# Kernel optimization log

Hardware: AMD Instinct MI355X
Metric: run time of the kernel (lower is better)

The kernel has to match this reference:

```python
import jax, jax.numpy as jnp
import numpy as np

IOU_THRESHOLD = 0.5
NEG_POS_RATIO = 3
CENTER_VARIANCE = 0.1
SIZE_VARIANCE = 0.2


def _corner_to_center(b):
    return jnp.concatenate([(b[..., :2] + b[..., 2:]) * 0.5, b[..., 2:] - b[..., :2]], axis=-1)


def _area(lt, rb):
    wh = jnp.clip(rb - lt, 0.0)
    return wh[..., 0] * wh[..., 1]


def _iou(boxes0, boxes1, eps=1e-5):
    lt = jnp.maximum(boxes0[..., :2], boxes1[..., :2])
    rb = jnp.minimum(boxes0[..., 2:], boxes1[..., 2:])
    inter = _area(lt, rb)
    a0 = _area(boxes0[..., :2], boxes0[..., 2:])
    a1 = _area(boxes1[..., :2], boxes1[..., 2:])
    return inter / (a0 + a1 - inter + eps)


def _match_one(gt_boxes, gt_labels, valid, anchors_corner, anchors_center):
    # gt_boxes [G,4] corner, gt_labels [G], valid [G] bool, anchors [A,4]
    G = gt_boxes.shape[0]
    A = anchors_corner.shape[0]
    ious = _iou(gt_boxes[:, None, :], anchors_corner[None, :, :])  # [G, A]
    ious = jnp.where(valid[:, None], ious, -1.0)  # mask padded gts
    best_target_iou = ious.max(axis=0)            # [A]
    best_target_idx = ious.argmax(axis=0)         # [A]
    best_prior_idx = ious.argmax(axis=1)          # [G]
    # force-assign each valid gt to its best anchor (invalid rows -> OOB, dropped)
    safe_prior = jnp.where(valid, best_prior_idx, A)
    best_target_idx = best_target_idx.at[safe_prior].set(jnp.arange(G), mode='drop')
    best_target_iou = best_target_iou.at[safe_prior].set(2.0, mode='drop')
    labels = jnp.where(best_target_iou < IOU_THRESHOLD, 0, gt_labels[best_target_idx])
    boxes_c = _corner_to_center(gt_boxes[best_target_idx])  # [A,4] center form
    loc = jnp.concatenate([
        (boxes_c[:, :2] - anchors_center[:, :2]) / anchors_center[:, 2:] / CENTER_VARIANCE,
        jnp.log(jnp.clip(boxes_c[:, 2:] / anchors_center[:, 2:], 1e-8)) / SIZE_VARIANCE,
    ], axis=-1)
    return labels, loc


def _multibox_loss(confidence, predicted_locations, gts, counts, anchors):
    B, A, C = confidence.shape
    G = gts.shape[1]
    gt_boxes = gts[..., :4]
    gt_labels = gts[..., 4].astype(jnp.int32)
    valid = jnp.arange(G)[None, :] < counts[:, None]  # [B, G]
    anchors_center = _corner_to_center(anchors)
    labels, gt_locations = jax.vmap(_match_one, in_axes=(0, 0, 0, None, None))(
        gt_boxes, gt_labels, valid, anchors, anchors_center)  # [B,A], [B,A,4]

    log_probs = jax.nn.log_softmax(confidence, axis=2)  # [B, A, C]
    bg_loss = -log_probs[:, :, 0]                       # [B, A]
    pos_mask = labels > 0
    num_pos_row = pos_mask.sum(axis=1, keepdims=True)   # [B, 1]
    # hard negative mining: rank background losses per row, keep top 3*num_pos
    mining = jnp.where(pos_mask, -jnp.inf, bg_loss)
    order = jnp.argsort(-mining, axis=1)
    rank = jnp.argsort(order, axis=1)
    neg_mask = rank < num_pos_row * NEG_POS_RATIO
    mask = pos_mask | neg_mask

    num_pos = jnp.maximum(1.0, pos_mask.sum().astype(confidence.dtype))
    ce = -jnp.take_along_axis(log_probs, labels[..., None], axis=2)[..., 0]  # [B, A]
    classification_loss = jnp.where(mask, ce, 0.0).sum() / (num_pos * 4.0)

    diff = jnp.abs(predicted_locations - gt_locations)
    smooth_l1 = jnp.where(diff < 1.0, 0.5 * diff * diff, diff - 0.5)
    localisation_loss = (smooth_l1 * pos_mask[..., None]).sum() / (num_pos * 4.0)
    return localisation_loss, classification_loss


def setup_inputs() -> dict:
    key = jax.random.key(0)
    ks = jax.random.split(key, 8)
    B, A, G, C = 32, 32768, 50, 22
    confidence = jax.random.normal(ks[0], (B, A, C), jnp.float32)
    predicted_locations = jax.random.normal(ks[1], (B, A, 4), jnp.float32)
    a_c = jax.random.uniform(ks[2], (A, 2), minval=0.05, maxval=0.95)
    a_wh = jax.random.uniform(ks[3], (A, 2), minval=0.02, maxval=0.3)
    anchors = jnp.concatenate([jnp.clip(a_c - a_wh * 0.5, 0.0, 1.0),
                               jnp.clip(a_c + a_wh * 0.5, 0.0, 1.0)], axis=-1)
    g_c = jax.random.uniform(ks[4], (B, G, 2), minval=0.1, maxval=0.9)
    g_wh = jax.random.uniform(ks[5], (B, G, 2), minval=0.05, maxval=0.4)
    g_boxes = jnp.concatenate([jnp.clip(g_c - g_wh * 0.5, 0.0, 1.0),
                               jnp.clip(g_c + g_wh * 0.5, 0.0, 1.0)], axis=-1)
    g_labels = jax.random.randint(ks[6], (B, G), 1, C).astype(jnp.float32)
    gts = jnp.concatenate([g_boxes, g_labels[..., None]], axis=-1)
    counts = jax.random.randint(ks[7], (B,), 1, G + 1).astype(jnp.int32)
    return {"confidence": confidence, "predicted_locations": predicted_locations,
            "gts": gts, "counts": counts, "anchors": anchors}


def reference(confidence, predicted_locations, gts, counts, anchors):
    return _multibox_loss(confidence, predicted_locations, gts, counts, anchors)
```

## Files before the change

### kernel.cpp

```cpp
#include <hip/hip_runtime.h>
#include <cstdint>
#include <cstddef>

#define B_N 32
#define A_N 32768
#define G_N 50
#define C_N 22
#define BA  (B_N * A_N)

#define GC 4
#define NCHUNK ((G_N + GC - 1) / GC)

#define SEL_CAP 4096


__device__ __forceinline__ float iou_one(float gx0, float gy0, float gx1, float gy1, float ga,
                                         float ax0, float ay0, float ax1, float ay1, float aa) {
    float lx = fmaxf(gx0, ax0), ly = fmaxf(gy0, ay0);
    float rx = fminf(gx1, ax1), ry = fminf(gy1, ay1);
    float iw = fmaxf(rx - lx, 0.0f), ih = fmaxf(ry - ly, 0.0f);
    float inter = iw * ih;
    return inter / (ga + aa - inter + 1e-5f);
}

__device__ __forceinline__ unsigned int f2key(float x) {
    unsigned int u = __float_as_uint(x);
    return (u & 0x80000000u) ? ~u : (u | 0x80000000u);
}

__device__ __forceinline__ float key2f(unsigned int k) {
    return __uint_as_float((k & 0x80000000u) ? (k & 0x7FFFFFFFu) : ~k);
}


__global__ void init_kernel(float* hdr) {
    if (threadIdx.x < 128) hdr[threadIdx.x] = 0.0f;
}

__global__ __launch_bounds__(256) void best_prior_kernel(
        const float* __restrict__ gts, const int* __restrict__ counts,
        const float* __restrict__ anchors, int* __restrict__ bp_idx) {
    int b  = blockIdx.x / NCHUNK;
    int ch = blockIdx.x % NCHUNK;
    int g0 = ch * GC;
    int cnt = counts[b];
    if (g0 >= cnt) return;
    int ng = cnt - g0; if (ng > GC) ng = GC;
    __shared__ float sg[GC][5];
    if (threadIdx.x < (unsigned)ng) {
        int g = g0 + threadIdx.x;
        const float* gtb = gts + (size_t)(b * G_N + g) * 5;
        float x0 = gtb[0], y0 = gtb[1], x1 = gtb[2], y1 = gtb[3];
        sg[threadIdx.x][0] = x0; sg[threadIdx.x][1] = y0;
        sg[threadIdx.x][2] = x1; sg[threadIdx.x][3] = y1;
        sg[threadIdx.x][4] = fmaxf(x1 - x0, 0.0f) * fmaxf(y1 - y0, 0.0f);
    }
    __syncthreads();
    float bv[GC]; int bi[GC];
    #pragma unroll
    for (int j = 0; j < GC; ++j) { bv[j] = -1e30f; bi[j] = 0; }
    for (int a = threadIdx.x; a < A_N; a += 256) {
        float4 an = reinterpret_cast<const float4*>(anchors)[a];
        float aa = fmaxf(an.z - an.x, 0.0f) * fmaxf(an.w - an.y, 0.0f);
        #pragma unroll
        for (int j = 0; j < GC; ++j) {
            float iou = iou_one(sg[j][0], sg[j][1], sg[j][2], sg[j][3], sg[j][4],
                                an.x, an.y, an.z, an.w, aa);
            if (iou > bv[j]) { bv[j] = iou; bi[j] = a; }
        }
    }
    __shared__ float sv[256];
    __shared__ int   si[256];
    for (int j = 0; j < ng; ++j) {
        sv[threadIdx.x] = bv[j]; si[threadIdx.x] = bi[j];
        __syncthreads();
        for (int s = 128; s > 0; s >>= 1) {
            if (threadIdx.x < s) {
                float v2 = sv[threadIdx.x + s]; int i2 = si[threadIdx.x + s];
                float v1 = sv[threadIdx.x];     int i1 = si[threadIdx.x];
                if (v2 > v1 || (v2 == v1 && i2 < i1)) { sv[threadIdx.x] = v2; si[threadIdx.x] = i2; }
            }
            __syncthreads();
        }
        if (threadIdx.x == 0) bp_idx[b * G_N + g0 + j] = si[0];
        __syncthreads();
    }
}

__global__ __launch_bounds__(256) void fused_kernel(
        const float* __restrict__ gts, const int* __restrict__ counts,
        const float* __restrict__ anchors, const float* __restrict__ pred_loc,
        const float* __restrict__ conf, const int* __restrict__ bp_idx,
        float* __restrict__ mining, float* __restrict__ loc_part,
        float* __restrict__ ce_part, int* __restrict__ num_pos_row) {
    int i = blockIdx.x * 256 + threadIdx.x;
    int b = blockIdx.x >> 7;
    int a = i & (A_N - 1);
    int cnt = counts[b];
    __shared__ float sg[G_N][5];
    __shared__ int   sl[G_N];
    __shared__ int   sp[G_N];
    if (threadIdx.x < G_N) {
        int g = threadIdx.x;
        const float* gtb = gts + (size_t)(b * G_N + g) * 5;
        float x0 = gtb[0], y0 = gtb[1], x1 = gtb[2], y1 = gtb[3];
        sg[g][0] = x0; sg[g][1] = y0; sg[g][2] = x1; sg[g][3] = y1;
        sg[g][4] = fmaxf(x1 - x0, 0.0f) * fmaxf(y1 - y0, 0.0f);
        sl[g] = (int)gtb[4];
        sp[g] = bp_idx[b * G_N + g];
    }
    __syncthreads();

    float4 an = reinterpret_cast<const float4*>(anchors)[a];
    float aa = fmaxf(an.z - an.x, 0.0f) * fmaxf(an.w - an.y, 0.0f);
    float best = -2.0f; int gi = 0;
    for (int g = 0; g < cnt; ++g) {
        float iou = iou_one(sg[g][0], sg[g][1], sg[g][2], sg[g][3], sg[g][4],
                            an.x, an.y, an.z, an.w, aa);
        if (iou > best) { best = iou; gi = g; }
    }
    bool forced = false;
    for (int g = 0; g < cnt; ++g) {
        if (sp[g] == a) { gi = g; forced = true; }
    }
    float iou_eff = forced ? 2.0f : best;
    int label = 0;
    if (!(iou_eff < 0.5f)) label = sl[gi];
    bool pos = label > 0;

    float contrib = 0.0f;
    if (pos) {
        float acx = (an.x + an.z) * 0.5f, acy = (an.y + an.w) * 0.5f;
        float aw = an.z - an.x, ah = an.w - an.y;
        float gx0 = sg[gi][0], gy0 = sg[gi][1], gx1 = sg[gi][2], gy1 = sg[gi][3];
        float cx = (gx0 + gx1) * 0.5f, cy = (gy0 + gy1) * 0.5f;
        float w = gx1 - gx0, h = gy1 - gy0;
        float l0 = ((cx - acx) / aw) / 0.1f;
        float l1 = ((cy - acy) / ah) / 0.1f;
        float l2 = logf(fmaxf(w / aw, 1e-8f)) / 0.2f;
        float l3 = logf(fmaxf(h / ah, 1e-8f)) / 0.2f;
        float4 p = reinterpret_cast<const float4*>(pred_loc)[i];
        float d0 = fabsf(p.x - l0), d1 = fabsf(p.y - l1);
        float d2 = fabsf(p.z - l2), d3 = fabsf(p.w - l3);
        contrib  = (d0 < 1.0f ? 0.5f * d0 * d0 : d0 - 0.5f);
        contrib += (d1 < 1.0f ? 0.5f * d1 * d1 : d1 - 0.5f);
        contrib += (d2 < 1.0f ? 0.5f * d2 * d2 : d2 - 0.5f);
        contrib += (d3 < 1.0f ? 0.5f * d3 * d3 : d3 - 0.5f);
    }

    float v[C_N];
    const float2* c2 = reinterpret_cast<const float2*>(conf + (size_t)i * C_N);
    #pragma unroll
    for (int j = 0; j < C_N / 2; ++j) { float2 t = c2[j]; v[2 * j] = t.x; v[2 * j + 1] = t.y; }
    float m = v[0];
    #pragma unroll
    for (int j = 1; j < C_N; ++j) m = fmaxf(m, v[j]);
    float s = 0.0f;
    #pragma unroll
    for (int j = 0; j < C_N; ++j) s += expf(v[j] - m);
    float ls = logf(s);
    float ce_pos = 0.0f;
    if (pos) {
        float vl = v[0];
        #pragma unroll
        for (int j = 1; j < C_N; ++j) vl = (j == label) ? v[j] : vl;
        ce_pos = ls - (vl - m);
        mining[i] = __int_as_float(0xFF800000);
    } else {
        mining[i] = ls - (v[0] - m);
    }

    unsigned long long bal = __ballot(pos);
    for (int o = 32; o > 0; o >>= 1) {
        contrib += __shfl_down(contrib, o, 64);
        ce_pos  += __shfl_down(ce_pos, o, 64);
    }
    __shared__ float swl[4], swc[4];
    __shared__ int   swi[4];
    int wid = threadIdx.x >> 6, lane = threadIdx.x & 63;
    if (lane == 0) { swl[wid] = contrib; swc[wid] = ce_pos; swi[wid] = __popcll(bal); }
    __syncthreads();
    if (threadIdx.x == 0) {
        float sL = swl[0] + swl[1] + swl[2] + swl[3];
        float sC = swc[0] + swc[1] + swc[2] + swc[3];
        int   c  = swi[0] + swi[1] + swi[2] + swi[3];
        int slot = blockIdx.x & 31;
        if (sL != 0.0f) atomicAdd(&loc_part[slot], sL);
        if (sC != 0.0f) atomicAdd(&ce_part[slot], sC);
        if (c) atomicAdd(&num_pos_row[b], c);
    }
}

__device__ __forceinline__ void scan_pick(unsigned* hist, int nwords,
                                          unsigned* sA, unsigned* sB,
                                          int krem, int* s_bin, int* s_krem) {
    int t = threadIdx.x;
    unsigned lo = 0, hi = 0;
    if (t < nwords) { unsigned w = hist[t]; lo = w & 0xFFFFu; hi = w >> 16; }
    sA[t] = lo + hi;
    __syncthreads();
    unsigned* src = sA; unsigned* dst = sB;
    for (int d = 1; d < 1024; d <<= 1) {
        unsigned vv = src[t] + ((t + d < 1024) ? src[t + d] : 0u);
        dst[t] = vv;
        __syncthreads();
        unsigned* tmp = src; src = dst; dst = tmp;
    }
    unsigned incl = src[t];
    unsigned incl_next = (t < 1023) ? src[t + 1] : 0u;
    unsigned uk = (unsigned)krem;
    if (incl >= uk && incl_next < uk) {
        unsigned cum = incl_next;
        if (cum + hi >= uk) { *s_bin = 2 * t + 1; *s_krem = (int)(uk - cum); }
        else                { *s_bin = 2 * t;     *s_krem = (int)(uk - cum - hi); }
    }
    __syncthreads();
}

__global__ __launch_bounds__(1024) void select_kernel(
        const float* __restrict__ mining, const int* __restrict__ num_pos_row,
        float* __restrict__ neg_sum) {
    int b = blockIdx.x;
    int tid = threadIdx.x;
    int np = num_pos_row[b];
    long long k = 3LL * np;
    int num_neg = A_N - np;
    int k_eff = (int)((k < (long long)num_neg) ? k : (long long)num_neg);
    if (k_eff <= 0) { if (tid == 0) neg_sum[b] = 0.0f; return; }
    const float4* row4 = reinterpret_cast<const float4*>(mining + (size_t)b * A_N);

    __shared__ unsigned hist[1024];
    __shared__ unsigned sA[1024], sB[1024];
    __shared__ unsigned surv[SEL_CAP];
    __shared__ int s_n1, s_bin, s_krem;
    __shared__ float swf[16];

    hist[tid] = 0;
    if (tid == 0) s_n1 = 0;
    __syncthreads();
    #pragma unroll
    for (int it = 0; it < A_N / 4 / 1024; ++it) {
        float4 vv = row4[tid + it * 1024];
        unsigned k0 = f2key(vv.x), k1 = f2key(vv.y), k2 = f2key(vv.z), k3 = f2key(vv.w);
        unsigned b0 = k0 >> 21, b1 = k1 >> 21, b2 = k2 >> 21, b3 = k3 >> 21;
        atomicAdd(&hist[b0 >> 1], (b0 & 1) ? 65536u : 1u);
        atomicAdd(&hist[b1 >> 1], (b1 & 1) ? 65536u : 1u);
        atomicAdd(&hist[b2 >> 1], (b2 & 1) ? 65536u : 1u);
        atomicAdd(&hist[b3 >> 1], (b3 & 1) ? 65536u : 1u);
    }
    __syncthreads();
    scan_pick(hist, 1024, sA, sB, k_eff, &s_bin, &s_krem);
    unsigned bin1 = (unsigned)s_bin;
    int krem1 = s_krem;
    __syncthreads();

    float sum_sel = 0.0f;
    #pragma unroll
    for (int it = 0; it < A_N / 4 / 1024; ++it) {
        float4 vv = row4[tid + it * 1024];
        float xs[4] = {vv.x, vv.y, vv.z, vv.w};
        #pragma unroll
        for (int e = 0; e < 4; ++e) {
            unsigned key = f2key(xs[e]);
            unsigned t11 = key >> 21;
            if (t11 > bin1) sum_sel += xs[e];
            else if (t11 == bin1) {
                int p = atomicAdd(&s_n1, 1);
                if (p < SEL_CAP) surv[p] = key;
            }
        }
    }
    __syncthreads();
    int n1 = s_n1;
    bool in_lds = (n1 <= SEL_CAP);

    hist[tid] = 0;
    __syncthreads();
    if (in_lds) {
        for (int ii = tid; ii < n1; ii += 1024) {
            unsigned bin = (surv[ii] >> 10) & 0x7FFu;
            atomicAdd(&hist[bin >> 1], (bin & 1) ? 65536u : 1u);
        }
    } else {
        for (int it = 0; it < A_N / 4 / 1024; ++it) {
            float4 vv = row4[tid + it * 1024];
            float xs[4] = {vv.x, vv.y, vv.z, vv.w};
            for (int e = 0; e < 4; ++e) {
                unsigned key = f2key(xs[e]);
                if ((key >> 21) == bin1) {
                    unsigned bin = (key >> 10) & 0x7FFu;
                    atomicAdd(&hist[bin >> 1], (bin & 1) ? 65536u : 1u);
                }
            }
        }
    }
    __syncthreads();
    scan_pick(hist, 1024, sA, sB, krem1, &s_bin, &s_krem);
    unsigned prefix22 = (bin1 << 11) | (unsigned)s_bin;
    int krem2 = s_krem;
    __syncthreads();

    hist[tid] = 0;
    __syncthreads();
    if (in_lds) {
        for (int ii = tid; ii < n1; ii += 1024) {
            unsigned key = surv[ii];
            if ((key >> 10) == prefix22) {
                unsigned bin = key & 0x3FFu;
                atomicAdd(&hist[bin >> 1], (bin & 1) ? 65536u : 1u);
            }
        }
    } else {
        for (int it = 0; it < A_N / 4 / 1024; ++it) {
            float4 vv = row4[tid + it * 1024];
            float xs[4] = {vv.x, vv.y, vv.z, vv.w};
            for (int e = 0; e < 4; ++e) {
                unsigned key = f2key(xs[e]);
                if ((key >> 10) == prefix22) {
                    unsigned bin = key & 0x3FFu;
                    atomicAdd(&hist[bin >> 1], (bin & 1) ? 65536u : 1u);
                }
            }
        }
    }
    __syncthreads();
    scan_pick(hist, 512, sA, sB, krem2, &s_bin, &s_krem);
    unsigned kth = (prefix22 << 10) | (unsigned)s_bin;
    int krem3 = s_krem;
    __syncthreads();

    if (in_lds) {
        for (int ii = tid; ii < n1; ii += 1024) {
            unsigned key = surv[ii];
            if (key > kth) sum_sel += key2f(key);
        }
    } else {
        for (int it = 0; it < A_N / 4 / 1024; ++it) {
            float4 vv = row4[tid + it * 1024];
            float xs[4] = {vv.x, vv.y, vv.z, vv.w};
            for (int e = 0; e < 4; ++e) {
                unsigned key = f2key(xs[e]);
                if ((key >> 21) == bin1 && key > kth) sum_sel += xs[e];
            }
        }
    }
    for (int o = 32; o > 0; o >>= 1) sum_sel += __shfl_down(sum_sel, o, 64);
    int wid = tid >> 6, lane = tid & 63;
    if (lane == 0) swf[wid] = sum_sel;
    __syncthreads();
    if (tid == 0) {
        float tot = 0.0f;
        #pragma unroll
        for (int w = 0; w < 16; ++w) tot += swf[w];
        neg_sum[b] = tot + (float)krem3 * key2f(kth);
    }
}

__global__ void final_kernel(const float* __restrict__ loc_part, const float* __restrict__ ce_part,
                             const int* __restrict__ num_pos_row, const float* __restrict__ neg_sum,
                             float* __restrict__ out) {
    if (threadIdx.x != 0) return;
    int tot = 0;
    for (int b = 0; b < B_N; ++b) tot += num_pos_row[b];
    float npos = fmaxf(1.0f, (float)tot);
    float L = 0.0f, Cp = 0.0f, Ng = 0.0f;
    for (int j = 0; j < B_N; ++j) { L += loc_part[j]; Cp += ce_part[j]; Ng += neg_sum[j]; }
    out[0] = L / (npos * 4.0f);
    out[1] = (Cp + Ng) / (npos * 4.0f);
}


extern "C" void kernel_launch(void* const* d_in, const int* in_sizes, int n_in,
                              void* d_out, int out_size, void* d_ws, size_t ws_size,
                              hipStream_t stream) {
    const float* conf     = (const float*)d_in[0];
    const float* pred_loc = (const float*)d_in[1];
    const float* gts      = (const float*)d_in[2];
    const int*   counts   = (const int*)d_in[3];
    const float* anchors  = (const float*)d_in[4];
    float* out = (float*)d_out;

    char* ws = (char*)d_ws;
    float* loc_part     = (float*)ws;
    float* ce_part      = (float*)(ws + 128);
    int*   num_pos_row  = (int*)(ws + 256);
    float* neg_sum      = (float*)(ws + 384);
    int*   bp_idx       = (int*)(ws + 512);
    float* mining       = (float*)(ws + 8192);

    init_kernel<<<1, 128, 0, stream>>>(loc_part);
    best_prior_kernel<<<B_N * NCHUNK, 256, 0, stream>>>(gts, counts, anchors, bp_idx);
    fused_kernel<<<BA / 256, 256, 0, stream>>>(gts, counts, anchors, pred_loc, conf, bp_idx,
                                               mining, loc_part, ce_part, num_pos_row);
    select_kernel<<<B_N, 1024, 0, stream>>>(mining, num_pos_row, neg_sum);
    final_kernel<<<1, 64, 0, stream>>>(loc_part, ce_part, num_pos_row, neg_sum, out);
}
```

Before: 301.2 us.

## Split best-prior search across anchor segments with packed 64-bit atomicMax

The best-prior argmax search is split across 16 anchor segments per GT chunk, giving 16x more blocks. Each block reduces IoU and inverted anchor index, packed into one 64-bit key, with wave shuffles and then a global atomicMax. The shared-memory tree reduction and its many barriers go away, and the tie-break still favours the lowest index. The cost is an init pass over the atomic buffer and more global atomics.

```diff
diff --git a/kernel.cpp b/kernel.cpp
--- a/kernel.cpp
+++ b/kernel.cpp
@@ -10,6 +10,8 @@
 
 #define GC 4
 #define NCHUNK ((G_N + GC - 1) / GC)
+#define ASEG 16
+#define ASEG_LEN (A_N / ASEG)
 
 #define SEL_CAP 4096
 
@@ -33,64 +35,64 @@
 }
 
 
-__global__ void init_kernel(float* hdr) {
+__global__ void init_kernel(float* hdr, unsigned long long* bp_best) {
     if (threadIdx.x < 128) hdr[threadIdx.x] = 0.0f;
+    for (int i = threadIdx.x; i < B_N * G_N; i += 256) bp_best[i] = 0ull;
 }
 
 __global__ __launch_bounds__(256) void best_prior_kernel(
         const float* __restrict__ gts, const int* __restrict__ counts,
-        const float* __restrict__ anchors, int* __restrict__ bp_idx) {
-    int b  = blockIdx.x / NCHUNK;
-    int ch = blockIdx.x % NCHUNK;
-    int g0 = ch * GC;
+        const float* __restrict__ anchors, unsigned long long* __restrict__ bp_best) {
+    int blk = blockIdx.x;
+    int b   = blk / (NCHUNK * ASEG);
+    int rem = blk % (NCHUNK * ASEG);
+    int ch  = rem / ASEG;
+    int seg = rem % ASEG;
+    int g0  = ch * GC;
     int cnt = counts[b];
     if (g0 >= cnt) return;
-    int ng = cnt - g0; if (ng > GC) ng = GC;
-    __shared__ float sg[GC][5];
-    if (threadIdx.x < (unsigned)ng) {
-        int g = g0 + threadIdx.x;
-        const float* gtb = gts + (size_t)(b * G_N + g) * 5;
-        float x0 = gtb[0], y0 = gtb[1], x1 = gtb[2], y1 = gtb[3];
-        sg[threadIdx.x][0] = x0; sg[threadIdx.x][1] = y0;
-        sg[threadIdx.x][2] = x1; sg[threadIdx.x][3] = y1;
-        sg[threadIdx.x][4] = fmaxf(x1 - x0, 0.0f) * fmaxf(y1 - y0, 0.0f);
-    }
-    __syncthreads();
-    float bv[GC]; int bi[GC];
-    #pragma unroll
-    for (int j = 0; j < GC; ++j) { bv[j] = -1e30f; bi[j] = 0; }
-    for (int a = threadIdx.x; a < A_N; a += 256) {
+    float gx0[GC], gy0[GC], gx1[GC], gy1[GC], ga[GC];
+    #pragma unroll
+    for (int j = 0; j < GC; ++j) {
+        if (g0 + j < cnt) {
+            const float* p = gts + (size_t)(b * G_N + g0 + j) * 5;
+            gx0[j] = p[0]; gy0[j] = p[1]; gx1[j] = p[2]; gy1[j] = p[3];
+            ga[j] = fmaxf(gx1[j] - gx0[j], 0.0f) * fmaxf(gy1[j] - gy0[j], 0.0f);
+        } else { gx0[j] = 0.f; gy0[j] = 0.f; gx1[j] = 0.f; gy1[j] = 0.f; ga[j] = 0.f; }
+    }
+    unsigned long long best[GC];
+    #pragma unroll
+    for (int j = 0; j < GC; ++j) best[j] = 0ull;
+    int a0 = seg * ASEG_LEN;
+    for (int a = a0 + threadIdx.x; a < a0 + ASEG_LEN; a += 256) {
         float4 an = reinterpret_cast<const float4*>(anchors)[a];
         float aa = fmaxf(an.z - an.x, 0.0f) * fmaxf(an.w - an.y, 0.0f);
         #pragma unroll
         for (int j = 0; j < GC; ++j) {
-            float iou = iou_one(sg[j][0], sg[j][1], sg[j][2], sg[j][3], sg[j][4],
+            float iou = iou_one(gx0[j], gy0[j], gx1[j], gy1[j], ga[j],
                                 an.x, an.y, an.z, an.w, aa);
-            if (iou > bv[j]) { bv[j] = iou; bi[j] = a; }
-        }
-    }
-    __shared__ float sv[256];
-    __shared__ int   si[256];
-    for (int j = 0; j < ng; ++j) {
-        sv[threadIdx.x] = bv[j]; si[threadIdx.x] = bi[j];
-        __syncthreads();
-        for (int s = 128; s > 0; s >>= 1) {
-            if (threadIdx.x < s) {
-                float v2 = sv[threadIdx.x + s]; int i2 = si[threadIdx.x + s];
-                float v1 = sv[threadIdx.x];     int i1 = si[threadIdx.x];
-                if (v2 > v1 || (v2 == v1 && i2 < i1)) { sv[threadIdx.x] = v2; si[threadIdx.x] = i2; }
-            }
-            __syncthreads();
-        }
-        if (threadIdx.x == 0) bp_idx[b * G_N + g0 + j] = si[0];
-        __syncthreads();
+            unsigned long long key = ((unsigned long long)f2key(iou) << 32) | (unsigned)(~a);
+            if (key > best[j]) best[j] = key;
+        }
+    }
+    #pragma unroll
+    for (int j = 0; j < GC; ++j) {
+        for (int o = 32; o > 0; o >>= 1) {
+            unsigned long long other = __shfl_down(best[j], o, 64);
+            if (other > best[j]) best[j] = other;
+        }
+    }
+    if ((threadIdx.x & 63) == 0) {
+        int ng = cnt - g0; if (ng > GC) ng = GC;
+        for (int j = 0; j < ng; ++j)
+            atomicMax(&bp_best[b * G_N + g0 + j], best[j]);
     }
 }
 
 __global__ __launch_bounds__(256) void fused_kernel(
         const float* __restrict__ gts, const int* __restrict__ counts,
         const float* __restrict__ anchors, const float* __restrict__ pred_loc,
-        const float* __restrict__ conf, const int* __restrict__ bp_idx,
+        const float* __restrict__ conf, const unsigned long long* __restrict__ bp_best,
         float* __restrict__ mining, float* __restrict__ loc_part,
         float* __restrict__ ce_part, int* __restrict__ num_pos_row) {
     int i = blockIdx.x * 256 + threadIdx.x;
@@ -107,7 +109,7 @@
         sg[g][0] = x0; sg[g][1] = y0; sg[g][2] = x1; sg[g][3] = y1;
         sg[g][4] = fmaxf(x1 - x0, 0.0f) * fmaxf(y1 - y0, 0.0f);
         sl[g] = (int)gtb[4];
-        sp[g] = bp_idx[b * G_N + g];
+        sp[g] = (int)(~(unsigned)(bp_best[b * G_N + g] & 0xFFFFFFFFull));
     }
     __syncthreads();
 
@@ -385,12 +387,12 @@
     float* ce_part      = (float*)(ws + 128);
     int*   num_pos_row  = (int*)(ws + 256);
     float* neg_sum      = (float*)(ws + 384);
-    int*   bp_idx       = (int*)(ws + 512);
-    float* mining       = (float*)(ws + 8192);
-
-    init_kernel<<<1, 128, 0, stream>>>(loc_part);
-    best_prior_kernel<<<B_N * NCHUNK, 256, 0, stream>>>(gts, counts, anchors, bp_idx);
-    fused_kernel<<<BA / 256, 256, 0, stream>>>(gts, counts, anchors, pred_loc, conf, bp_idx,
+    unsigned long long* bp_best = (unsigned long long*)(ws + 512);
+    float* mining       = (float*)(ws + 16384);
+
+    init_kernel<<<1, 256, 0, stream>>>(loc_part, bp_best);
+    best_prior_kernel<<<B_N * NCHUNK * ASEG, 256, 0, stream>>>(gts, counts, anchors, bp_best);
+    fused_kernel<<<BA / 256, 256, 0, stream>>>(gts, counts, anchors, pred_loc, conf, bp_best,
                                                mining, loc_part, ce_part, num_pos_row);
     select_kernel<<<B_N, 1024, 0, stream>>>(mining, num_pos_row, neg_sum);
     final_kernel<<<1, 64, 0, stream>>>(loc_part, ce_part, num_pos_row, neg_sum, out);
```

Result: faster. 253.4 us (-15.9%).
